# Optimization experiments

Measured on AMD Instinct MI355X. Metric: run time of the kernel, lower is better.

## Reference

```python
import jax, jax.numpy as jnp
import numpy as np
from math import sqrt

EMBED_DIM = 1024
NUM_HEADS = 16
HEAD_DIM = EMBED_DIM // NUM_HEADS  # 64
SCALE = sqrt(HEAD_DIM)


def _rotate_half(x):
    # matches torch: stack((-x[...,1::2], x[...,0::2]), -1).flatten(-2)
    x1 = x[..., 0::2]
    x2 = x[..., 1::2]
    return jnp.stack((-x2, x1), axis=-1).reshape(x.shape)


def _apply_rope(x, seq_len):
    # x: [B, H, S, D]
    inv_freq = 1.0 / (10000.0 ** (jnp.arange(0, HEAD_DIM, 2, dtype=jnp.float32) / HEAD_DIM))
    pos = jnp.arange(seq_len, dtype=jnp.float32)
    freqs = jnp.outer(pos, inv_freq)            # [S, D/2]
    emb = jnp.concatenate([freqs, freqs], -1)   # [S, D]
    cos = jnp.cos(emb)[None, None].astype(x.dtype)
    sin = jnp.sin(emb)[None, None].astype(x.dtype)
    return x * cos + _rotate_half(x) * sin


def setup_inputs() -> dict:
    key = jax.random.key(0)
    ks = jax.random.split(key, 9)
    B, S, E = 2, 2048, EMBED_DIM
    s = 1.0 / np.sqrt(E)
    return {
        "x": jax.random.normal(ks[0], (B, S, E), jnp.float32),
        "Wq": jax.random.uniform(ks[1], (E, E), jnp.float32, -s, s),
        "bq": jnp.zeros((E,), jnp.float32),
        "Wk": jax.random.uniform(ks[2], (E, E), jnp.float32, -s, s),
        "bk": jnp.zeros((E,), jnp.float32),
        "Wv": jax.random.uniform(ks[3], (E, E), jnp.float32, -s, s),
        "bv": jnp.zeros((E,), jnp.float32),
        "Wo": jax.random.uniform(ks[4], (E, E), jnp.float32, -s, s),
        "bo": jnp.zeros((E,), jnp.float32),
    }


def reference(x, Wq, bq, Wk, bk, Wv, bv, Wo, bo):
    B, S, E = x.shape
    H, D = NUM_HEADS, HEAD_DIM
    # projections (torch Linear: x @ W.T + b), split heads -> [B, H, S, D]
    q = (x @ Wq.T + bq).reshape(B, S, H, D).transpose(0, 2, 1, 3)
    k = (x @ Wk.T + bk).reshape(B, S, H, D).transpose(0, 2, 1, 3)
    v = (x @ Wv.T + bv).reshape(B, S, H, D).transpose(0, 2, 1, 3)
    q = _apply_rope(q, S)
    k = _apply_rope(k, S)
    attn = jnp.einsum("bhqd,bhkd->bhqk", q, k) / SCALE
    attn = jax.nn.softmax(attn, axis=-1)
    out = jnp.einsum("bhqk,bhkd->bhqd", attn, v)
    out = out.transpose(0, 2, 1, 3).reshape(B, S, E)
    return out @ Wo.T + bo
```

## Files before the change

kernel.cpp:

```cpp
#include <hip/hip_runtime.h>
#include <hip/hip_bf16.h>
#include <math.h>

typedef __bf16 bf16;
typedef __bf16 bf16x4 __attribute__((ext_vector_type(4)));
typedef __bf16 bf16x8 __attribute__((ext_vector_type(8)));
typedef float f32x4 __attribute__((ext_vector_type(4)));

#define SEQ  2048
#define EMB  1024
#define NH   16
#define HD   64
#define MTOT 4096

__device__ __forceinline__ void gl_lds16(const void* g, void* l) {
  __builtin_amdgcn_global_load_lds(
      (const __attribute__((address_space(1))) void*)g,
      (__attribute__((address_space(3))) void*)l, 16, 0, 0);
}

__device__ __forceinline__ f32x4 mfma16(bf16x8 a, bf16x8 b, f32x4 c) {
  return __builtin_amdgcn_mfma_f32_16x16x32_bf16(a, b, c, 0, 0, 0);
}

#define ROPE_C 0.41524101186092026f
#define QSCL  0.1803368801111244f

__global__ __launch_bounds__(256) void cvt_all_kernel(
    const float* __restrict__ x,
    const float* __restrict__ w0, const float* __restrict__ w1,
    const float* __restrict__ w2, const float* __restrict__ w3,
    bf16* __restrict__ dst) {
  const int y = blockIdx.y;
  const size_t WN = (size_t)EMB * EMB;
  const float* src = (y < 4) ? (x + (size_t)y * WN)
                   : (y == 4) ? w0 : (y == 5) ? w1 : (y == 6) ? w2 : w3;
  size_t i = ((size_t)blockIdx.x * 256 + threadIdx.x) * 8;
  float4 a = *(const float4*)(src + i);
  float4 b = *(const float4*)(src + i + 4);
  bf16x8 o;
  o[0] = (bf16)a.x; o[1] = (bf16)a.y; o[2] = (bf16)a.z; o[3] = (bf16)a.w;
  o[4] = (bf16)b.x; o[5] = (bf16)b.y; o[6] = (bf16)b.z; o[7] = (bf16)b.w;
  *(bf16x8*)(dst + (size_t)y * WN + i) = o;
}

__global__ __launch_bounds__(256) void gemm_kernel(
    const bf16* __restrict__ X,
    const bf16* __restrict__ W0, const bf16* __restrict__ W1, const bf16* __restrict__ W2,
    const float* __restrict__ B0, const float* __restrict__ B1, const float* __restrict__ B2,
    bf16* __restrict__ Oq, bf16* __restrict__ Ok, bf16* __restrict__ Ovt)
{
  const int K = EMB;
  const int tid  = threadIdx.x;
  const int lane = tid & 63;
  const int w    = tid >> 6;
  const int wm   = w >> 1, wn = w & 1;
  const int lin = blockIdx.x + blockIdx.y * 8;
  const int sw  = (lin & 7) * 32 + (lin >> 3);
  const int tile_n = (sw & 7) * 128;
  const int tile_m = (sw >> 3) * 128;
  const int z = blockIdx.z;
  const bf16*  Wsel = (z == 0) ? W0 : (z == 1 ? W1 : W2);
  const float* Bsel = (z == 0) ? B0 : (z == 1 ? B1 : B2);

  __shared__ __align__(16) unsigned char smem[33792];
  bf16* As = (bf16*)smem;
  bf16* Bs = (bf16*)(smem + 16384);

  f32x4 acc[4][4];
#pragma unroll
  for (int i = 0; i < 4; i++)
#pragma unroll
    for (int j = 0; j < 4; j++) acc[i][j] = f32x4{0.f, 0.f, 0.f, 0.f};

  const int quad  = lane >> 4;
  const int l15   = lane & 15;
  const int srow8 = lane >> 3;
  const int p8    = lane & 7;
  const int csrc  = p8 ^ srow8;

  for (int k0 = 0; k0 < K; k0 += 64) {
#pragma unroll
    for (int i = 0; i < 4; i++) {
      const int ii = w * 4 + i;
      const int r  = ii * 8 + srow8;
      gl_lds16(X    + (size_t)(tile_m + r) * K + k0 + csrc * 8, As + ii * 512);
      gl_lds16(Wsel + (size_t)(tile_n + r) * K + k0 + csrc * 8, Bs + ii * 512);
    }
    __syncthreads();

#pragma unroll
    for (int kk = 0; kk < 2; kk++) {
      bf16x8 af[4], bfr[4];
#pragma unroll
      for (int mt = 0; mt < 4; mt++) {
        int ml = wm * 64 + mt * 16 + l15;
        af[mt] = *(const bf16x8*)(As + ml * 64 + (((kk * 4 + quad) ^ (ml & 7)) & 7) * 8);
      }
#pragma unroll
      for (int nt = 0; nt < 4; nt++) {
        int nl = wn * 64 + nt * 16 + l15;
        bfr[nt] = *(const bf16x8*)(Bs + nl * 64 + (((kk * 4 + quad) ^ (nl & 7)) & 7) * 8);
      }
#pragma unroll
      for (int mt = 0; mt < 4; mt++)
#pragma unroll
        for (int nt = 0; nt < 4; nt++)
          acc[mt][nt] = mfma16(af[mt], bfr[nt], acc[mt][nt]);
    }
    __syncthreads();
  }

  bf16* CS = (bf16*)smem;
  const int b = tile_m >> 11;
  const int s0 = tile_m & (SEQ - 1);

  if (z < 2) {
#pragma unroll
    for (int nt = 0; nt < 4; nt++) {
      const int nl = wn * 64 + nt * 16 + l15;
      const int n = tile_n + nl;
      const float bias = Bsel[n];
      const int j = n & 31;
      const float invf = exp2f(-(float)j * ROPE_C);
#pragma unroll
      for (int mt = 0; mt < 4; mt++) {
#pragma unroll
        for (int r = 0; r < 4; r++) {
          const int ml = wm * 64 + mt * 16 + quad * 4 + r;
          float a = acc[mt][nt][r] + bias;
          float p = __shfl_xor(a, 1, 64);
          float th = (float)(s0 + ml) * invf;
          float sn, cs;
          __sincosf(th, &sn, &cs);
          float res = (n & 1) ? fmaf(p, sn, a * cs) : fmaf(-p, sn, a * cs);
          if (z == 0) res *= QSCL;
          CS[ml * 132 + nl] = (bf16)res;
        }
      }
    }
    __syncthreads();
    bf16* Odst = (z == 0) ? Oq : Ok;
#pragma unroll
    for (int g = 0; g < 8; g++) {
      int unit = g * 256 + tid;
      int chunk = unit & 7;
      int row = unit >> 3;
      int hl = row >> 7, sl = row & 127;
      bf16x8 v = *(const bf16x8*)(CS + sl * 132 + hl * 64 + chunk * 8);
      int hg = (tile_n >> 6) + hl;
      size_t o = ((size_t)(b * NH + hg) * SEQ + s0 + sl) * HD + chunk * 8;
      *(bf16x8*)(Odst + o) = v;
    }
  } else {
#pragma unroll
    for (int nt = 0; nt < 4; nt++) {
      const int nl = wn * 64 + nt * 16 + l15;
      const float bias = Bsel[tile_n + nl];
#pragma unroll
      for (int mt = 0; mt < 4; mt++) {
        const int mb = wm * 64 + mt * 16 + quad * 4;
#pragma unroll
        for (int r = 0; r < 4; r++) {
          const int ml = mb + r;
          const int mp = (ml & ~31) | ((ml & 12) << 1) | ((ml & 16) >> 2) | (ml & 3);
          CS[nl * 132 + mp] = (bf16)(acc[mt][nt][r] + bias);
        }
      }
    }
    __syncthreads();
#pragma unroll
    for (int g = 0; g < 8; g++) {
      int unit = g * 256 + tid;
      int chunk = unit & 15;
      int row = unit >> 4;
      bf16x8 v = *(const bf16x8*)(CS + row * 132 + chunk * 8);
      int nglob = tile_n + row;
      int d = nglob & 63, hg = nglob >> 6;
      size_t o = ((size_t)(b * NH + hg) * HD + d) * SEQ + s0 + chunk * 8;
      *(bf16x8*)(Ovt + o) = v;
    }
  }
}

__global__ __launch_bounds__(256) void gemm_o_kernel(
    const bf16* __restrict__ X,
    const bf16* __restrict__ W,
    const float* __restrict__ Bb,
    float* __restrict__ Out)
{
  const int tid = threadIdx.x, lane = tid & 63, w = tid >> 6;
  const int lin = blockIdx.x + blockIdx.y * 8;
  const int sw  = (lin & 7) * 64 + (lin >> 3);
  const int tile_n = (sw & 7) * 128;
  const int tile_m = (sw >> 3) * 64;
  __shared__ __align__(16) bf16 As[64 * 64];
  __shared__ __align__(16) bf16 Bs[128 * 64];

  f32x4 acc[4][2];
#pragma unroll
  for (int i = 0; i < 4; i++)
#pragma unroll
    for (int j = 0; j < 2; j++) acc[i][j] = f32x4{0.f, 0.f, 0.f, 0.f};

  const int quad = lane >> 4, l15 = lane & 15;
  const int srow8 = lane >> 3, p8 = lane & 7;
  const int csrc = p8 ^ srow8;

  for (int k0 = 0; k0 < EMB; k0 += 64) {
#pragma unroll
    for (int i = 0; i < 2; i++) {
      const int ii = w * 2 + i;
      const int r  = ii * 8 + srow8;
      gl_lds16(X + (size_t)(tile_m + r) * EMB + k0 + csrc * 8, As + ii * 512);
    }
#pragma unroll
    for (int i = 0; i < 4; i++) {
      const int ii = w * 4 + i;
      const int r  = ii * 8 + srow8;
      gl_lds16(W + (size_t)(tile_n + r) * EMB + k0 + csrc * 8, Bs + ii * 512);
    }
    __syncthreads();

#pragma unroll
    for (int kk = 0; kk < 2; kk++) {
      bf16x8 af[4], bfr[2];
#pragma unroll
      for (int mt = 0; mt < 4; mt++) {
        int ml = mt * 16 + l15;
        af[mt] = *(const bf16x8*)(As + ml * 64 + (((kk * 4 + quad) ^ (ml & 7)) & 7) * 8);
      }
#pragma unroll
      for (int nt = 0; nt < 2; nt++) {
        int nl = w * 32 + nt * 16 + l15;
        bfr[nt] = *(const bf16x8*)(Bs + nl * 64 + (((kk * 4 + quad) ^ (nl & 7)) & 7) * 8);
      }
#pragma unroll
      for (int mt = 0; mt < 4; mt++)
#pragma unroll
        for (int nt = 0; nt < 2; nt++)
          acc[mt][nt] = mfma16(af[mt], bfr[nt], acc[mt][nt]);
    }
    __syncthreads();
  }

#pragma unroll
  for (int nt = 0; nt < 2; nt++) {
    const int n = tile_n + w * 32 + nt * 16 + l15;
    const float bias = Bb[n];
#pragma unroll
    for (int mt = 0; mt < 4; mt++) {
#pragma unroll
      for (int r = 0; r < 4; r++) {
        const int m = tile_m + mt * 16 + quad * 4 + r;
        Out[(size_t)m * EMB + n] = acc[mt][nt][r] + bias;
      }
    }
  }
}

__global__ __launch_bounds__(256) void flash_kernel(
    const bf16* __restrict__ Q,
    const bf16* __restrict__ Kk,
    const bf16* __restrict__ Vt,
    bf16* __restrict__ O)
{
  const int lin = blockIdx.x + blockIdx.y * 16;
  const int sw  = (lin & 7) * 64 + (lin >> 3);
  const int bh  = sw >> 4;
  const int qt  = sw & 15;
  const int tid = threadIdx.x, lane = tid & 63, w = tid >> 6;
  const int quad = lane >> 4, l15 = lane & 15;

  __shared__ __align__(16) unsigned char smem[65536];

  const bf16* qbase = Q  + (size_t)bh * SEQ * HD;
  const bf16* kbase = Kk + (size_t)bh * SEQ * HD;
  const bf16* vbase = Vt + (size_t)bh * HD * SEQ;

  auto stage = [&](int kt, int buf) {
    bf16* Ks = (bf16*)(smem + buf * 32768);
    bf16* Vs = Ks + 8192;
#pragma unroll
    for (int i = 0; i < 4; i++) {
      int r = w * 32 + i * 8 + (lane >> 3);
      int c = (lane & 7) ^ (r & 7);
      gl_lds16(kbase + (size_t)(kt * 128 + r) * HD + c * 8, Ks + (w * 32 + i * 8) * 64);
      int dv = w * 16 + i * 4 + (lane >> 4);
      int cv = (lane & 15) ^ (dv & 15);
      gl_lds16(vbase + (size_t)dv * SEQ + kt * 128 + cv * 8, Vs + (w * 16 + i * 4) * 128);
    }
  };

  stage(0, 0);

  bf16x8 qf[2][2];
#pragma unroll
  for (int m = 0; m < 2; m++)
#pragma unroll
    for (int t = 0; t < 2; t++)
      qf[m][t] = *(const bf16x8*)(qbase + (size_t)(qt * 128 + w * 32 + m * 16 + l15) * HD
                                  + t * 32 + quad * 8);

  bf16x8 ones;
#pragma unroll
  for (int i = 0; i < 8; i++) ones[i] = (bf16)1.0f;

  f32x4 lacc[2];
  f32x4 oacc[2][4];
#pragma unroll
  for (int m = 0; m < 2; m++) {
    lacc[m] = f32x4{0.f, 0.f, 0.f, 0.f};
#pragma unroll
    for (int i = 0; i < 4; i++) oacc[m][i] = f32x4{0.f, 0.f, 0.f, 0.f};
  }

  __syncthreads();

  for (int kt = 0; kt < SEQ / 128; kt++) {
    const int buf = kt & 1;
    if (kt + 1 < SEQ / 128) stage(kt + 1, buf ^ 1);
    const bf16* Ks = (const bf16*)(smem + buf * 32768);
    const bf16* Vs = Ks + 8192;

    __builtin_amdgcn_s_setprio(1);
#pragma unroll
    for (int t2 = 0; t2 < 4; t2++) {
      bf16x8 pa[2];
#pragma unroll
      for (int hh = 0; hh < 2; hh++) {
        const int krow = (t2 * 2 + hh) * 16 + l15;
        const int swz = krow & 7;
        bf16x8 kf0 = *(const bf16x8*)(Ks + krow * 64 + ((quad ^ swz) & 7) * 8);
        bf16x8 kf1 = *(const bf16x8*)(Ks + krow * 64 + (((4 + quad) ^ swz) & 7) * 8);
#pragma unroll
        for (int mq = 0; mq < 2; mq++) {
          f32x4 s = f32x4{0.f, 0.f, 0.f, 0.f};
          s = mfma16(kf0, qf[mq][0], s);
          s = mfma16(kf1, qf[mq][1], s);
#pragma unroll
          for (int r = 0; r < 4; r++)
            pa[mq][hh * 4 + r] = (bf16)__builtin_amdgcn_exp2f(s[r]);
        }
      }
#pragma unroll
      for (int dt = 0; dt < 4; dt++) {
        const int d = dt * 16 + l15;
        bf16x8 vv = *(const bf16x8*)(Vs + d * 128 + ((t2 * 4 + quad) ^ l15) * 8);
#pragma unroll
        for (int mq = 0; mq < 2; mq++)
          oacc[mq][dt] = mfma16(vv, pa[mq], oacc[mq][dt]);
      }
#pragma unroll
      for (int mq = 0; mq < 2; mq++)
        lacc[mq] = mfma16(ones, pa[mq], lacc[mq]);
    }
    __builtin_amdgcn_s_setprio(0);
    __syncthreads();
  }

  float rls[2];
#pragma unroll
  for (int mq = 0; mq < 2; mq++)
    rls[mq] = __builtin_amdgcn_rcpf(lacc[mq][0]);

  const int b = bh >> 4, h = bh & 15;
#pragma unroll
  for (int mq = 0; mq < 2; mq++) {
    const int srow = qt * 128 + w * 32 + mq * 16 + l15;
    bf16* orow = O + ((size_t)(b * SEQ + srow)) * EMB + h * HD;
#pragma unroll
    for (int dt = 0; dt < 4; dt++) {
      bf16x4 ov;
#pragma unroll
      for (int r = 0; r < 4; r++) ov[r] = (bf16)(oacc[mq][dt][r] * rls[mq]);
      *(bf16x4*)(orow + dt * 16 + quad * 4) = ov;
    }
  }
}

extern "C" void kernel_launch(void* const* d_in, const int* in_sizes, int n_in,
                              void* d_out, int out_size, void* d_ws, size_t ws_size,
                              hipStream_t stream) {
  const float* x  = (const float*)d_in[0];
  const float* Wq = (const float*)d_in[1];
  const float* bq = (const float*)d_in[2];
  const float* Wk = (const float*)d_in[3];
  const float* bk = (const float*)d_in[4];
  const float* Wv = (const float*)d_in[5];
  const float* bv = (const float*)d_in[6];
  const float* Wo = (const float*)d_in[7];
  const float* bo = (const float*)d_in[8];

  const size_t XN = (size_t)MTOT * EMB;
  const size_t WN = (size_t)EMB * EMB;

  bf16* xb = (bf16*)d_ws;
  bf16* wq = xb + XN;
  bf16* wk = wq + WN;
  bf16* wv = wk + WN;
  bf16* wo = wv + WN;
  bf16* q  = wo + WN;
  bf16* k  = q + XN;
  bf16* vt = k + XN;
  bf16* at = vt + XN;
  float* out = (float*)d_out;

  dim3 blk(256);
  cvt_all_kernel<<<dim3(512, 8), blk, 0, stream>>>(x, Wq, Wk, Wv, Wo, xb);

  gemm_kernel<<<dim3(8, 32, 3), blk, 0, stream>>>(
      xb, wq, wk, wv, bq, bk, bv, q, k, vt);
  flash_kernel<<<dim3(16, 32), blk, 0, stream>>>(q, k, vt, at);
  gemm_o_kernel<<<dim3(8, 64), blk, 0, stream>>>(at, wo, bo, out);
}
```

Measured before the change: 189.7 us.

## Halve flash tiles to 64 rows for more blocks and precompute RoPE table

```diff
diff --git a/kernel.cpp b/kernel.cpp
--- a/kernel.cpp
+++ b/kernel.cpp
@@ -25,6 +25,16 @@
 
 #define ROPE_C 0.41524101186092026f
 #define QSCL  0.1803368801111244f
+
+__global__ __launch_bounds__(256) void rope_tab_kernel(float2* __restrict__ tab) {
+  int idx = blockIdx.x * 256 + threadIdx.x;
+  int s = idx >> 5, j = idx & 31;
+  float invf = exp2f(-(float)j * ROPE_C);
+  float th = (float)s * invf;
+  float sn, cs;
+  __sincosf(th, &sn, &cs);
+  tab[idx] = make_float2(cs, sn);
+}
 
 __global__ __launch_bounds__(256) void cvt_all_kernel(
     const float* __restrict__ x,
@@ -48,6 +58,7 @@
     const bf16* __restrict__ X,
     const bf16* __restrict__ W0, const bf16* __restrict__ W1, const bf16* __restrict__ W2,
     const float* __restrict__ B0, const float* __restrict__ B1, const float* __restrict__ B2,
+    const float2* __restrict__ tab,
     bf16* __restrict__ Oq, bf16* __restrict__ Ok, bf16* __restrict__ Ovt)
 {
   const int K = EMB;
@@ -122,7 +133,6 @@
       const int n = tile_n + nl;
       const float bias = Bsel[n];
       const int j = n & 31;
-      const float invf = exp2f(-(float)j * ROPE_C);
 #pragma unroll
       for (int mt = 0; mt < 4; mt++) {
 #pragma unroll
@@ -130,10 +140,8 @@
           const int ml = wm * 64 + mt * 16 + quad * 4 + r;
           float a = acc[mt][nt][r] + bias;
           float p = __shfl_xor(a, 1, 64);
-          float th = (float)(s0 + ml) * invf;
-          float sn, cs;
-          __sincosf(th, &sn, &cs);
-          float res = (n & 1) ? fmaf(p, sn, a * cs) : fmaf(-p, sn, a * cs);
+          const float2 t = tab[((s0 + ml) << 5) + j];
+          float res = (n & 1) ? fmaf(p, t.y, a * t.x) : fmaf(-p, t.y, a * t.x);
           if (z == 0) res *= QSCL;
           CS[ml * 132 + nl] = (bf16)res;
         }
@@ -265,117 +273,96 @@
     const bf16* __restrict__ Vt,
     bf16* __restrict__ O)
 {
-  const int lin = blockIdx.x + blockIdx.y * 16;
-  const int sw  = (lin & 7) * 64 + (lin >> 3);
-  const int bh  = sw >> 4;
-  const int qt  = sw & 15;
+  const int lin = blockIdx.x + blockIdx.y * 32;
+  const int sw  = (lin & 7) * 128 + (lin >> 3);
+  const int bh  = sw >> 5;
+  const int qt  = sw & 31;
   const int tid = threadIdx.x, lane = tid & 63, w = tid >> 6;
   const int quad = lane >> 4, l15 = lane & 15;
 
-  __shared__ __align__(16) unsigned char smem[65536];
+  __shared__ __align__(16) unsigned char smem[32768];
 
   const bf16* qbase = Q  + (size_t)bh * SEQ * HD;
   const bf16* kbase = Kk + (size_t)bh * SEQ * HD;
   const bf16* vbase = Vt + (size_t)bh * HD * SEQ;
 
   auto stage = [&](int kt, int buf) {
-    bf16* Ks = (bf16*)(smem + buf * 32768);
-    bf16* Vs = Ks + 8192;
-#pragma unroll
-    for (int i = 0; i < 4; i++) {
-      int r = w * 32 + i * 8 + (lane >> 3);
+    bf16* Ks = (bf16*)(smem + buf * 16384);
+    bf16* Vs = Ks + 4096;
+#pragma unroll
+    for (int i = 0; i < 2; i++) {
+      int r = w * 16 + i * 8 + (lane >> 3);
       int c = (lane & 7) ^ (r & 7);
-      gl_lds16(kbase + (size_t)(kt * 128 + r) * HD + c * 8, Ks + (w * 32 + i * 8) * 64);
-      int dv = w * 16 + i * 4 + (lane >> 4);
-      int cv = (lane & 15) ^ (dv & 15);
-      gl_lds16(vbase + (size_t)dv * SEQ + kt * 128 + cv * 8, Vs + (w * 16 + i * 4) * 128);
+      gl_lds16(kbase + (size_t)(kt * 64 + r) * HD + c * 8, Ks + (w * 16 + i * 8) * 64);
+      gl_lds16(vbase + (size_t)r * SEQ + kt * 64 + c * 8, Vs + (w * 16 + i * 8) * 64);
     }
   };
 
   stage(0, 0);
 
-  bf16x8 qf[2][2];
-#pragma unroll
-  for (int m = 0; m < 2; m++)
-#pragma unroll
-    for (int t = 0; t < 2; t++)
-      qf[m][t] = *(const bf16x8*)(qbase + (size_t)(qt * 128 + w * 32 + m * 16 + l15) * HD
-                                  + t * 32 + quad * 8);
+  bf16x8 qf[2];
+#pragma unroll
+  for (int t = 0; t < 2; t++)
+    qf[t] = *(const bf16x8*)(qbase + (size_t)(qt * 64 + w * 16 + l15) * HD
+                             + t * 32 + quad * 8);
 
   bf16x8 ones;
 #pragma unroll
   for (int i = 0; i < 8; i++) ones[i] = (bf16)1.0f;
 
-  f32x4 lacc[2];
-  f32x4 oacc[2][4];
-#pragma unroll
-  for (int m = 0; m < 2; m++) {
-    lacc[m] = f32x4{0.f, 0.f, 0.f, 0.f};
-#pragma unroll
-    for (int i = 0; i < 4; i++) oacc[m][i] = f32x4{0.f, 0.f, 0.f, 0.f};
-  }
+  f32x4 lacc = f32x4{0.f, 0.f, 0.f, 0.f};
+  f32x4 oacc[4];
+#pragma unroll
+  for (int i = 0; i < 4; i++) oacc[i] = f32x4{0.f, 0.f, 0.f, 0.f};
 
   __syncthreads();
 
-  for (int kt = 0; kt < SEQ / 128; kt++) {
+  for (int kt = 0; kt < SEQ / 64; kt++) {
     const int buf = kt & 1;
-    if (kt + 1 < SEQ / 128) stage(kt + 1, buf ^ 1);
-    const bf16* Ks = (const bf16*)(smem + buf * 32768);
-    const bf16* Vs = Ks + 8192;
+    if (kt + 1 < SEQ / 64) stage(kt + 1, buf ^ 1);
+    const bf16* Ks = (const bf16*)(smem + buf * 16384);
+    const bf16* Vs = Ks + 4096;
 
     __builtin_amdgcn_s_setprio(1);
 #pragma unroll
-    for (int t2 = 0; t2 < 4; t2++) {
-      bf16x8 pa[2];
+    for (int t2 = 0; t2 < 2; t2++) {
+      bf16x8 pa;
 #pragma unroll
       for (int hh = 0; hh < 2; hh++) {
         const int krow = (t2 * 2 + hh) * 16 + l15;
         const int swz = krow & 7;
         bf16x8 kf0 = *(const bf16x8*)(Ks + krow * 64 + ((quad ^ swz) & 7) * 8);
         bf16x8 kf1 = *(const bf16x8*)(Ks + krow * 64 + (((4 + quad) ^ swz) & 7) * 8);
-#pragma unroll
-        for (int mq = 0; mq < 2; mq++) {
-          f32x4 s = f32x4{0.f, 0.f, 0.f, 0.f};
-          s = mfma16(kf0, qf[mq][0], s);
-          s = mfma16(kf1, qf[mq][1], s);
-#pragma unroll
-          for (int r = 0; r < 4; r++)
-            pa[mq][hh * 4 + r] = (bf16)__builtin_amdgcn_exp2f(s[r]);
-        }
+        f32x4 s = f32x4{0.f, 0.f, 0.f, 0.f};
+        s = mfma16(kf0, qf[0], s);
+        s = mfma16(kf1, qf[1], s);
+#pragma unroll
+        for (int r = 0; r < 4; r++)
+          pa[hh * 4 + r] = (bf16)__builtin_amdgcn_exp2f(s[r]);
       }
 #pragma unroll
       for (int dt = 0; dt < 4; dt++) {
         const int d = dt * 16 + l15;
-        bf16x8 vv = *(const bf16x8*)(Vs + d * 128 + ((t2 * 4 + quad) ^ l15) * 8);
-#pragma unroll
-        for (int mq = 0; mq < 2; mq++)
-          oacc[mq][dt] = mfma16(vv, pa[mq], oacc[mq][dt]);
-      }
-#pragma unroll
-      for (int mq = 0; mq < 2; mq++)
-        lacc[mq] = mfma16(ones, pa[mq], lacc[mq]);
+        bf16x8 vv = *(const bf16x8*)(Vs + d * 64 + (((t2 * 4 + quad) ^ (d & 7)) & 7) * 8);
+        oacc[dt] = mfma16(vv, pa, oacc[dt]);
+      }
+      lacc = mfma16(ones, pa, lacc);
     }
     __builtin_amdgcn_s_setprio(0);
     __syncthreads();
   }
 
-  float rls[2];
-#pragma unroll
-  for (int mq = 0; mq < 2; mq++)
-    rls[mq] = __builtin_amdgcn_rcpf(lacc[mq][0]);
+  const float rls = __builtin_amdgcn_rcpf(lacc[0]);
 
   const int b = bh >> 4, h = bh & 15;
-#pragma unroll
-  for (int mq = 0; mq < 2; mq++) {
-    const int srow = qt * 128 + w * 32 + mq * 16 + l15;
-    bf16* orow = O + ((size_t)(b * SEQ + srow)) * EMB + h * HD;
-#pragma unroll
-    for (int dt = 0; dt < 4; dt++) {
-      bf16x4 ov;
-#pragma unroll
-      for (int r = 0; r < 4; r++) ov[r] = (bf16)(oacc[mq][dt][r] * rls[mq]);
-      *(bf16x4*)(orow + dt * 16 + quad * 4) = ov;
-    }
+  const int srow = qt * 64 + w * 16 + l15;
+  bf16* orow = O + ((size_t)(b * SEQ + srow)) * EMB + h * HD;
+#pragma unroll
+  for (int dt = 0; dt < 4; dt++) {
+    bf16x4 ov;
+#pragma unroll
+    for (int r = 0; r < 4; r++) ov[r] = (bf16)(oacc[dt][r] * rls);
+    *(bf16x4*)(orow + dt * 16 + quad * 4) = ov;
   }
 }
 
@@ -404,13 +391,15 @@
   bf16* k  = q + XN;
   bf16* vt = k + XN;
   bf16* at = vt + XN;
+  float2* tab = (float2*)(at + XN);
   float* out = (float*)d_out;
 
   dim3 blk(256);
+  rope_tab_kernel<<<dim3(256), blk, 0, stream>>>(tab);
   cvt_all_kernel<<<dim3(512, 8), blk, 0, stream>>>(x, Wq, Wk, Wv, Wo, xb);
 
   gemm_kernel<<<dim3(8, 32, 3), blk, 0, stream>>>(
-      xb, wq, wk, wv, bq, bk, bv, q, k, vt);
-  flash_kernel<<<dim3(16, 32), blk, 0, stream>>>(q, k, vt, at);
+      xb, wq, wk, wv, bq, bk, bv, tab, q, k, vt);
+  flash_kernel<<<dim3(32, 32), blk, 0, stream>>>(q, k, vt, at);
   gemm_o_kernel<<<dim3(8, 64), blk, 0, stream>>>(at, wo, bo, out);
 }
```

New measurement: 203.7 us. +7.4%, slower.

## Double K-step in output GEMM and stage epilogue through LDS for vector stores

Applied to the files above, without the earlier changes.

```diff
diff --git a/kernel.cpp b/kernel.cpp
--- a/kernel.cpp
+++ b/kernel.cpp
@@ -194,8 +194,9 @@
   const int sw  = (lin & 7) * 64 + (lin >> 3);
   const int tile_n = (sw & 7) * 128;
   const int tile_m = (sw >> 3) * 64;
-  __shared__ __align__(16) bf16 As[64 * 64];
-  __shared__ __align__(16) bf16 Bs[128 * 64];
+  __shared__ __align__(16) unsigned char smem[49152];
+  bf16* As = (bf16*)smem;
+  bf16* Bs = (bf16*)(smem + 16384);
 
   f32x4 acc[4][2];
 #pragma unroll
@@ -204,36 +205,37 @@
     for (int j = 0; j < 2; j++) acc[i][j] = f32x4{0.f, 0.f, 0.f, 0.f};
 
   const int quad = lane >> 4, l15 = lane & 15;
-  const int srow8 = lane >> 3, p8 = lane & 7;
-  const int csrc = p8 ^ srow8;
-
-  for (int k0 = 0; k0 < EMB; k0 += 64) {
-#pragma unroll
-    for (int i = 0; i < 2; i++) {
-      const int ii = w * 2 + i;
-      const int r  = ii * 8 + srow8;
-      gl_lds16(X + (size_t)(tile_m + r) * EMB + k0 + csrc * 8, As + ii * 512);
-    }
+  const int srow4 = lane >> 4;
+  const int p16   = lane & 15;
+  const int csrc_base = p16;
+
+  for (int k0 = 0; k0 < EMB; k0 += 128) {
 #pragma unroll
     for (int i = 0; i < 4; i++) {
-      const int ii = w * 4 + i;
-      const int r  = ii * 8 + srow8;
-      gl_lds16(W + (size_t)(tile_n + r) * EMB + k0 + csrc * 8, Bs + ii * 512);
-    }
-    __syncthreads();
-
-#pragma unroll
-    for (int kk = 0; kk < 2; kk++) {
+      int r = (w * 4 + i) * 4 + srow4;
+      int c = csrc_base ^ (r & 15);
+      gl_lds16(X + (size_t)(tile_m + r) * EMB + k0 + c * 8, As + (w * 4 + i) * 512);
+    }
+#pragma unroll
+    for (int i = 0; i < 8; i++) {
+      int r = (w * 8 + i) * 4 + srow4;
+      int c = csrc_base ^ (r & 15);
+      gl_lds16(W + (size_t)(tile_n + r) * EMB + k0 + c * 8, Bs + (w * 8 + i) * 512);
+    }
+    __syncthreads();
+
+#pragma unroll
+    for (int kk = 0; kk < 4; kk++) {
       bf16x8 af[4], bfr[2];
 #pragma unroll
       for (int mt = 0; mt < 4; mt++) {
         int ml = mt * 16 + l15;
-        af[mt] = *(const bf16x8*)(As + ml * 64 + (((kk * 4 + quad) ^ (ml & 7)) & 7) * 8);
+        af[mt] = *(const bf16x8*)(As + ml * 128 + (((kk * 4 + quad) ^ (ml & 15)) & 15) * 8);
       }
 #pragma unroll
       for (int nt = 0; nt < 2; nt++) {
         int nl = w * 32 + nt * 16 + l15;
-        bfr[nt] = *(const bf16x8*)(Bs + nl * 64 + (((kk * 4 + quad) ^ (nl & 7)) & 7) * 8);
+        bfr[nt] = *(const bf16x8*)(Bs + nl * 128 + (((kk * 4 + quad) ^ (nl & 15)) & 15) * 8);
       }
 #pragma unroll
       for (int mt = 0; mt < 4; mt++)
@@ -244,18 +246,25 @@
     __syncthreads();
   }
 
+  float* CSf = (float*)smem;
 #pragma unroll
   for (int nt = 0; nt < 2; nt++) {
-    const int n = tile_n + w * 32 + nt * 16 + l15;
-    const float bias = Bb[n];
-#pragma unroll
-    for (int mt = 0; mt < 4; mt++) {
-#pragma unroll
-      for (int r = 0; r < 4; r++) {
-        const int m = tile_m + mt * 16 + quad * 4 + r;
-        Out[(size_t)m * EMB + n] = acc[mt][nt][r] + bias;
-      }
-    }
+    const int nl = w * 32 + nt * 16 + l15;
+    const float bias = Bb[tile_n + nl];
+#pragma unroll
+    for (int mt = 0; mt < 4; mt++)
+#pragma unroll
+      for (int r = 0; r < 4; r++)
+        CSf[(mt * 16 + quad * 4 + r) * 132 + nl] = acc[mt][nt][r] + bias;
+  }
+  __syncthreads();
+#pragma unroll
+  for (int g = 0; g < 8; g++) {
+    int unit = g * 256 + tid;
+    int chunk = unit & 31;
+    int row = unit >> 5;
+    float4 v = *(const float4*)(CSf + row * 132 + chunk * 4);
+    *(float4*)(Out + (size_t)(tile_m + row) * EMB + tile_n + chunk * 4) = v;
   }
 }
 
```

After: 190.7 us. About the same (+0.5%).
